# Kernel optimization log

Hardware: AMD Instinct MI355X
Metric: run time of the kernel (lower is better)

Reference implementation:

```python
import jax, jax.numpy as jnp
import numpy as np

N_NODES = 100000
N_EDGES = 500000
FEAT = 128
HID = 256
N_ETYPES = 249
N_LINKS = 16384


def _lin_init(key, out_dim, in_dim, bias=True):
    k1, k2 = jax.random.split(key)
    bound = 1.0 / np.sqrt(in_dim)
    w = jax.random.uniform(k1, (out_dim, in_dim), jnp.float32, -bound, bound)
    if bias:
        b = jax.random.uniform(k2, (out_dim,), jnp.float32, -bound, bound)
        return w, b
    return w


def setup_inputs() -> dict:
    key = jax.random.key(0)
    ks = jax.random.split(key, 24)
    x = jax.random.normal(ks[0], (N_NODES, FEAT), jnp.float32)
    edge_index = jax.random.randint(ks[1], (2, N_EDGES), 0, N_NODES, jnp.int64)
    edge_type = jax.random.randint(ks[2], (N_EDGES,), 0, N_ETYPES, jnp.int64)
    src_idx = jax.random.randint(ks[3], (N_LINKS,), 0, N_NODES, jnp.int64)
    dst_idx = jax.random.randint(ks[4], (N_LINKS,), 0, N_NODES, jnp.int64)

    w_emb, b_emb = _lin_init(ks[5], HID, FEAT)
    edge_table = jax.random.normal(ks[6], (N_ETYPES, HID), jnp.float32)
    wl0, bl0 = _lin_init(ks[7], HID, HID)
    wr0 = _lin_init(ks[8], HID, HID, bias=False)
    we0, be0 = _lin_init(ks[9], HID, HID)
    wl1, bl1 = _lin_init(ks[10], HID, HID)
    wr1 = _lin_init(ks[11], HID, HID, bias=False)
    we1, be1 = _lin_init(ks[12], HID, HID)
    wp1, bp1 = _lin_init(ks[13], HID, 4 * HID)
    wp2, bp2 = _lin_init(ks[14], 1, HID)
    return dict(x=x, edge_index=edge_index, edge_type=edge_type,
                src_idx=src_idx, dst_idx=dst_idx,
                w_emb=w_emb, b_emb=b_emb, edge_table=edge_table,
                wl0=wl0, bl0=bl0, wr0=wr0, we0=we0, be0=be0,
                wl1=wl1, bl1=bl1, wr1=wr1, we1=we1, be1=be1,
                wp1=wp1, bp1=bp1, wp2=wp2, bp2=bp2)


def _sage_layer(h, src, dst, deg, wl, bl, wr):
    # mean aggregation over incoming edges + self loop (add_self_loops)
    nb_sum = jax.ops.segment_sum(h[src], dst, num_segments=N_NODES)  # [N,H]
    mean = (nb_sum + h) / (deg + 1.0)[:, None]
    return mean @ wl.T + bl + h @ wr.T  # lin_l(mean) + lin_r(x)


def reference(x, edge_index, edge_type, src_idx, dst_idx,
              w_emb, b_emb, edge_table,
              wl0, bl0, wr0, we0, be0,
              wl1, bl1, wr1, we1, be1,
              wp1, bp1, wp2, bp2):
    src, dst = edge_index[0], edge_index[1]
    deg = jax.ops.segment_sum(jnp.ones((src.shape[0],), jnp.float32), dst,
                              num_segments=N_NODES)  # in-degree (no self loop)
    h = x @ w_emb.T + b_emb  # node_embedding
    edge_emb = edge_table[edge_type]  # [E,H]
    # edge_lin outputs are discarded by SAGEConv (matches torch behavior)
    _ = edge_emb @ we0.T + be0
    _ = edge_emb @ we1.T + be1
    h = jax.nn.relu(_sage_layer(h, src, dst, deg, wl0, bl0, wr0))
    h = jax.nn.relu(_sage_layer(h, src, dst, deg, wl1, bl1, wr1))
    s, d = h[src_idx], h[dst_idx]
    combined = jnp.concatenate([s, d, s * d, jnp.abs(s - d)], axis=1)  # [B,4H]
    hidden = jax.nn.relu(combined @ wp1.T + bp1)
    logits = hidden @ wp2.T + bp2  # [B,1]
    return jax.nn.sigmoid(logits).squeeze()
```

## Files before the change

kernel.cpp:

```cpp
#include <hip/hip_runtime.h>
#include <hip/hip_bf16.h>
#include <cstdint>
#include <type_traits>

#define N_NODES 100000
#define N_EDGES 500000
#define FEAT 128
#define HID 256
#define N_LINKS 16384
#define BCAP 32

typedef __attribute__((ext_vector_type(8))) short short8;
typedef __attribute__((ext_vector_type(4))) float floatx4;
typedef __attribute__((ext_vector_type(16))) float floatx16;

__device__ __forceinline__ float ldf(const float* p) { return *p; }
__device__ __forceinline__ float ldf(const __hip_bfloat16* p) { return __bfloat162float(*p); }
__device__ __forceinline__ void stf(float* p, float v) { *p = v; }
__device__ __forceinline__ void stf(__hip_bfloat16* p, float v) { *p = __float2bfloat16(v); }

__device__ __forceinline__ void load4(const __hip_bfloat16* p, float v[4]) {
    const uint2 q = *(const uint2*)p;
    v[0] = __uint_as_float(q.x << 16);
    v[1] = __uint_as_float(q.x & 0xffff0000u);
    v[2] = __uint_as_float(q.y << 16);
    v[3] = __uint_as_float(q.y & 0xffff0000u);
}
__device__ __forceinline__ void store4(__hip_bfloat16* p, const float v[4]) {
    __hip_bfloat16 b[4];
    b[0] = __float2bfloat16(v[0]); b[1] = __float2bfloat16(v[1]);
    b[2] = __float2bfloat16(v[2]); b[3] = __float2bfloat16(v[3]);
    *(uint2*)p = *(const uint2*)b;
}

__device__ __forceinline__ void load8(const __hip_bfloat16* p, float v[8]) {
    const uint4 q = *(const uint4*)p;
    v[0] = __uint_as_float(q.x << 16);
    v[1] = __uint_as_float(q.x & 0xffff0000u);
    v[2] = __uint_as_float(q.y << 16);
    v[3] = __uint_as_float(q.y & 0xffff0000u);
    v[4] = __uint_as_float(q.z << 16);
    v[5] = __uint_as_float(q.z & 0xffff0000u);
    v[6] = __uint_as_float(q.w << 16);
    v[7] = __uint_as_float(q.w & 0xffff0000u);
}
__device__ __forceinline__ void store8(__hip_bfloat16* p, const float v[8]) {
    __hip_bfloat16 b[8];
    #pragma unroll
    for (int i = 0; i < 8; i++) b[i] = __float2bfloat16(v[i]);
    *(uint4*)p = *(const uint4*)b;
}

__device__ __forceinline__ void unpack8(const uint4& q, float v[8]) {
    v[0] = __uint_as_float(q.x << 16);
    v[1] = __uint_as_float(q.x & 0xffff0000u);
    v[2] = __uint_as_float(q.y << 16);
    v[3] = __uint_as_float(q.y & 0xffff0000u);
    v[4] = __uint_as_float(q.z << 16);
    v[5] = __uint_as_float(q.z & 0xffff0000u);
    v[6] = __uint_as_float(q.w << 16);
    v[7] = __uint_as_float(q.w & 0xffff0000u);
}

__device__ __forceinline__ void acc8(const uint4& q, float a[8]) {
    a[0] += __uint_as_float(q.x << 16);
    a[1] += __uint_as_float(q.x & 0xffff0000u);
    a[2] += __uint_as_float(q.y << 16);
    a[3] += __uint_as_float(q.y & 0xffff0000u);
    a[4] += __uint_as_float(q.z << 16);
    a[5] += __uint_as_float(q.z & 0xffff0000u);
    a[6] += __uint_as_float(q.w << 16);
    a[7] += __uint_as_float(q.w & 0xffff0000u);
}

__device__ __forceinline__ void gload_lds16(const short* g, short* lds) {
    __builtin_amdgcn_global_load_lds(
        reinterpret_cast<const __attribute__((address_space(1))) unsigned int*>(
            reinterpret_cast<uintptr_t>(g)),
        reinterpret_cast<__attribute__((address_space(3))) unsigned int*>(
            reinterpret_cast<uintptr_t>(lds)),
        16, 0, 0);
}

__device__ __forceinline__ int clampi(int v, int n) { return ((unsigned)v < (unsigned)n) ? v : 0; }


__global__ void zero_f32(float* p, int n) {
    int i = blockIdx.x * blockDim.x + threadIdx.x;
    if (i < n) p[i] = 0.0f;
}

__global__ void init_misc(int* __restrict__ deg, int* __restrict__ h0pad,
                          int* __restrict__ h1pad) {
    int i = blockIdx.x * blockDim.x + threadIdx.x;
    if (i < N_NODES) deg[i] = 0;
    if (i < 128) { h0pad[i] = 0; h1pad[i] = 0; }
}

__global__ void cvt_x(const float4* __restrict__ x, __hip_bfloat16* __restrict__ xb, int n4) {
    int i = blockIdx.x * blockDim.x + threadIdx.x;
    if (i >= n4) return;
    float4 v = x[i];
    float a[4] = {v.x, v.y, v.z, v.w};
    store4(&xb[(size_t)i * 4], a);
}

#define POF_EMB 0
#define POF_L0  32768
#define POF_R0  98304
#define POF_L1  163840
#define POF_R1  229376
#define POF_P1  294912
#define WP_ALL  557056
__global__ void cvt_wall(const float* __restrict__ w_emb, const float* __restrict__ wl0,
                         const float* __restrict__ wr0, const float* __restrict__ wl1,
                         const float* __restrict__ wr1, const float* __restrict__ wp1,
                         __hip_bfloat16* __restrict__ wbp) {
    int i = blockIdx.x * blockDim.x + threadIdx.x;
    if (i >= WP_ALL) return;
    const float* src; int off, ks;
    if      (i < POF_L0) { src = w_emb; off = POF_EMB; ks = 128; }
    else if (i < POF_R0) { src = wl0;   off = POF_L0;  ks = 256; }
    else if (i < POF_L1) { src = wr0;   off = POF_R0;  ks = 256; }
    else if (i < POF_R1) { src = wl1;   off = POF_L1;  ks = 256; }
    else if (i < POF_P1) { src = wr1;   off = POF_R1;  ks = 256; }
    else                 { src = wp1;   off = POF_P1;  ks = 1024; }
    int o = i - off;
    int kseg = o >> 11;
    int rem  = o & 2047;
    int n = rem >> 3, j = rem & 7;
    wbp[i] = __float2bfloat16(src[n * ks + kseg * 8 + j]);
}


__global__ void fill_buckets(const int* __restrict__ src, const int* __restrict__ dst,
                             int* __restrict__ deg, int* __restrict__ ebuf, int nE) {
    int e = blockIdx.x * blockDim.x + threadIdx.x;
    if (e >= nE) return;
    int d = clampi(dst[e], N_NODES);
    int pos = atomicAdd(&deg[d], 1);
    if (pos < BCAP) ebuf[d * BCAP + pos] = clampi(src[e], N_NODES);
}

__global__ void sort_rows(const int* __restrict__ deg, int* __restrict__ ebuf) {
    int n = blockIdx.x * blockDim.x + threadIdx.x;
    if (n >= N_NODES) return;
    int dg = deg[n]; if (dg > BCAP) dg = BCAP;
    int start = n * BCAP, end = start + dg;
    for (int i = start + 1; i < end; i++) {
        int key = ebuf[i];
        int j = i - 1;
        while (j >= start && ebuf[j] > key) { ebuf[j + 1] = ebuf[j]; j--; }
        ebuf[j + 1] = key;
    }
}


__global__ __launch_bounds__(256) void gather_agg(const __hip_bfloat16* __restrict__ h,
                                                  const int* __restrict__ deg,
                                                  const int* __restrict__ ebuf,
                                                  __hip_bfloat16* __restrict__ agg) {
    int wave = threadIdx.x >> 6, lane = threadIdx.x & 63;
    int half = lane >> 5, l32 = lane & 31;
    int n = blockIdx.x * 8 + wave * 2 + half;
    bool active = (n < N_NODES);
    int nn = active ? n : 0;
    int dg = active ? deg[nn] : 0;
    int dgc = dg > BCAP ? BCAP : dg;
    int start = nn * BCAP;
    int end = start + dgc;

    float acc[8];
    {
        float sv[8];
        load8(&h[(long long)nn * HID + l32 * 8], sv);
        #pragma unroll
        for (int k = 0; k < 8; k++) acc[k] = sv[k];
    }

    for (int e = start; e < end; e += 8) {
        int cnt = end - e;
        uint4 raw[8];
        #pragma unroll
        for (int i = 0; i < 8; i++) {
            int t = e + i; t = (t < end) ? t : (end - 1);
            int idx = ebuf[t];
            int s = (i < cnt) ? idx : N_NODES;
            raw[i] = *(const uint4*)&h[(long long)s * HID + l32 * 8];
        }
        #pragma unroll
        for (int i = 0; i < 8; i++) acc8(raw[i], acc);
    }

    float inv = 1.0f / (float)(dg + 1);
    #pragma unroll
    for (int k = 0; k < 8; k++) acc[k] *= inv;
    if (active) store8(&agg[(long long)n * HID + l32 * 8], acc);
}


template <int KS, bool DUAL, typename TC, bool RELU>
__global__ __launch_bounds__(256, 2) void gemm_kc(const __hip_bfloat16* __restrict__ A1,
                                                  const __hip_bfloat16* __restrict__ A2,
                                                  const __hip_bfloat16* __restrict__ Bp1,
                                                  const __hip_bfloat16* __restrict__ Bp2,
                                                  const float* __restrict__ bias,
                                                  TC* __restrict__ C, int M, int GX) {
    const int N = 256;
    const int NSTEP = (DUAL ? 2 : 1) * KS / 64;
    __shared__ __align__(16) short As[2][128 * 64];
    __shared__ __align__(16) short Bs[2][64 * 128];

    const int tid = threadIdx.x;
    const int w = tid >> 6, lane = tid & 63;
    const int half = lane >> 5, l32 = lane & 31;
    const int cg = blockIdx.y;

    const short* A1s = (const short*)A1;
    const short* A2s = (const short*)A2;
    const short* B1s = (const short*)Bp1;
    const short* B2s = (const short*)Bp2;

    const int NT = (M + 127) / 128;
    for (int tile = blockIdx.x; tile < NT; tile += GX) {
        const int row0 = tile * 128;

        auto stage = [&](int buf, int t) {
            const short* Asrc; const short* Bsrc; int kl;
            if (!DUAL || t < KS / 64) { Asrc = A1s; Bsrc = B1s; kl = t * 64; }
            else                      { Asrc = A2s; Bsrc = B2s; kl = t * 64 - KS; }
            #pragma unroll
            for (int i = 0; i < 4; i++) {
                int idx = i * 256 + tid;
                int row = idx >> 3, b16 = idx & 7;
                int gr = row0 + row; if (gr >= M) gr = M - 1;
                gload_lds16(Asrc + (size_t)gr * KS + kl + ((b16 ^ (row & 7)) * 8),
                            (short*)&As[buf][idx * 8]);
            }
            #pragma unroll
            for (int i = 0; i < 4; i++) {
                int idx = i * 256 + tid;
                int kseg = idx >> 7, col = idx & 127;
                gload_lds16(Bsrc + ((size_t)((kl >> 3) + kseg) * 256 + cg * 128 + col) * 8,
                            (short*)&Bs[buf][idx * 8]);
            }
        };

        floatx16 acc[4] = {};
        int cur = 0;
        stage(0, 0);
        __syncthreads();

        for (int t = 0; t < NSTEP; t++) {
            if (t + 1 < NSTEP) stage(cur ^ 1, t + 1);

            const int arow = w * 32 + l32;
            #pragma unroll
            for (int k16 = 0; k16 < 4; k16++) {
                int e = k16 * 2 + half;
                short8 a = *(const short8*)&As[cur][(arow * 8 + (e ^ (l32 & 7))) * 8];
                #pragma unroll
                for (int ct = 0; ct < 4; ct++) {
                    short8 b = *(const short8*)&Bs[cur][(e * 128 + ct * 32 + l32) * 8];
                    acc[ct] = __builtin_amdgcn_mfma_f32_32x32x16_bf16(a, b, acc[ct], 0, 0, 0);
                }
            }
            __syncthreads();
            cur ^= 1;
        }

        #pragma unroll
        for (int ct = 0; ct < 4; ct++) {
            int c = cg * 128 + ct * 32 + l32;
            float bc = bias[c];
            #pragma unroll
            for (int reg = 0; reg < 16; reg++) {
                int rr = row0 + w * 32 + (reg & 3) + 8 * (reg >> 2) + 4 * half;
                if (rr < M) {
                    float v = acc[ct][reg] + bc;
                    if (RELU) v = fmaxf(v, 0.0f);
                    stf(&C[(size_t)rr * N + c], v);
                }
            }
        }
    }
}


__global__ __launch_bounds__(256, 3) void pred_gemm(const __hip_bfloat16* __restrict__ h,
                                                    const int* __restrict__ src_idx,
                                                    const int* __restrict__ dst_idx,
                                                    const __hip_bfloat16* __restrict__ Bp,
                                                    const float* __restrict__ bias,
                                                    float* __restrict__ C, int M) {
    const int N = 256;
    __shared__ __align__(16) short Bs[2][16 * 64 * 8];

    int w = threadIdx.x >> 6, lane = threadIdx.x & 63;
    int quad = lane >> 4, l16 = lane & 15;
    int cg = blockIdx.y;
    int row0 = blockIdx.x * 64 + w * 16;

    const short* Bps = (const short*)Bp;

    int rr = row0 + l16;
    int r = rr < M ? rr : M - 1;
    int sidx = clampi(src_idx[r], N_NODES);
    int didx = clampi(dst_idx[r], N_NODES);

    uint4 sraw[8], draw[8];
    #pragma unroll
    for (int j = 0; j < 8; j++) {
        sraw[j] = *(const uint4*)&h[(size_t)sidx * HID + quad * 8 + j * 32];
        draw[j] = *(const uint4*)&h[(size_t)didx * HID + quad * 8 + j * 32];
    }

    auto stageB = [&](int buf, int chunk) {
        #pragma unroll
        for (int i = 0; i < 4; i++) {
            int idx = i * 256 + (int)threadIdx.x;
            int ks = idx >> 6, col = idx & 63;
            gload_lds16(Bps + ((size_t)(chunk * 16 + ks) * 256 + cg * 64 + col) * 8,
                        (short*)&Bs[buf][idx * 8]);
        }
    };

    floatx4 acc[4] = {};
    stageB(0, 0);
    __syncthreads();
    int cur = 0;

    #pragma unroll
    for (int c = 0; c < 8; c++) {
        if (c + 1 < 8) stageB(cur ^ 1, c + 1);

        #pragma unroll
        for (int s = 0; s < 4; s++) {
            const int j = ((c & 1) ? 4 : 0) + s;
            short8 a;
            if (c < 2) {
                a = *(const short8*)&sraw[j];
            } else if (c < 4) {
                a = *(const short8*)&draw[j];
            } else {
                float sv[8], dv[8];
                unpack8(sraw[j], sv);
                unpack8(draw[j], dv);
                __hip_bfloat16 b8[8];
                if (c < 6) {
                    #pragma unroll
                    for (int q = 0; q < 8; q++) b8[q] = __float2bfloat16(sv[q] * dv[q]);
                } else {
                    #pragma unroll
                    for (int q = 0; q < 8; q++) b8[q] = __float2bfloat16(fabsf(sv[q] - dv[q]));
                }
                a = *(const short8*)b8;
            }
            #pragma unroll
            for (int ct = 0; ct < 4; ct++) {
                short8 b = *(const short8*)&Bs[cur][((s * 4 + quad) * 64 + ct * 16 + l16) * 8];
                acc[ct] = __builtin_amdgcn_mfma_f32_16x16x32_bf16(a, b, acc[ct], 0, 0, 0);
            }
        }
        __syncthreads();
        cur ^= 1;
    }

    #pragma unroll
    for (int ct = 0; ct < 4; ct++) {
        int c = cg * 64 + ct * 16 + l16;
        float bc = bias[c];
        #pragma unroll
        for (int i = 0; i < 4; i++) {
            int r2 = row0 + quad * 4 + i;
            if (r2 < M) C[(size_t)r2 * N + c] = fmaxf(acc[ct][i] + bc, 0.0f);
        }
    }
}

__global__ __launch_bounds__(256) void pred_final(const float* __restrict__ hidden,
                                                  const float* __restrict__ wp2,
                                                  const float* __restrict__ bp2,
                                                  float* __restrict__ out) {
    int wave = threadIdx.x >> 6;
    int lane = threadIdx.x & 63;
    int row = blockIdx.x * 4 + wave;
    if (row >= N_LINKS) return;
    const float4 hv = *(const float4*)&hidden[(long long)row * HID + lane * 4];
    const float4 wv = *(const float4*)&wp2[lane * 4];
    float v = hv.x * wv.x + hv.y * wv.y + hv.z * wv.z + hv.w * wv.w;
    #pragma unroll
    for (int off = 32; off > 0; off >>= 1) v += __shfl_down(v, off, 64);
    if (lane == 0) out[row] = 1.0f / (1.0f + expf(-(v + bp2[0])));
}


extern "C" void kernel_launch(void* const* d_in, const int* in_sizes, int n_in,
                              void* d_out, int out_size, void* d_ws, size_t ws_size,
                              hipStream_t stream) {
    const float* x          = (const float*)d_in[0];
    const int*   edge_index = (const int*)d_in[1];
    const int*   e_src      = edge_index;
    const int*   e_dst      = edge_index + N_EDGES;
    const int*   src_idx    = (const int*)d_in[3];
    const int*   dst_idx    = (const int*)d_in[4];
    const float* w_emb      = (const float*)d_in[5];
    const float* b_emb      = (const float*)d_in[6];
    const float* wl0        = (const float*)d_in[8];
    const float* bl0        = (const float*)d_in[9];
    const float* wr0        = (const float*)d_in[10];
    const float* wl1        = (const float*)d_in[13];
    const float* bl1        = (const float*)d_in[14];
    const float* wr1        = (const float*)d_in[15];
    const float* wp1        = (const float*)d_in[18];
    const float* bp1        = (const float*)d_in[19];
    const float* wp2        = (const float*)d_in[20];
    const float* bp2        = (const float*)d_in[21];
    float* out = (float*)d_out;

    typedef __hip_bfloat16 bf16;
    const size_t NH  = (size_t)N_NODES * HID;
    const size_t NH1 = (size_t)(N_NODES + 1) * HID;

    char* p = (char*)d_ws;
    bf16* h0   = (bf16*)p;  p += NH1 * 2;
    bf16* h1   = (bf16*)p;  p += NH1 * 2;
    bf16* agg  = (bf16*)p;  p += NH * 2;
    bf16* xb   = (bf16*)p;  p += (size_t)N_NODES * FEAT * 2;
    bf16* wbp  = (bf16*)p;  p += (size_t)WP_ALL * 2;
    p = (char*)(((uintptr_t)p + 255) & ~(uintptr_t)255);
    int* deg  = (int*)p; p += (size_t)N_NODES * 4;
    int* ebuf = (int*)p; p += (size_t)N_NODES * BCAP * 4;
    const size_t need = (size_t)(p - (char*)d_ws);

    if (ws_size < need) {
        zero_f32<<<(out_size + 255) / 256, 256, 0, stream>>>(out, out_size);
        return;
    }

    float* hidden = (float*)h1;

    init_misc<<<(N_NODES + 255) / 256, 256, 0, stream>>>(
        deg, (int*)(h0 + NH), (int*)(h1 + NH));
    fill_buckets<<<(N_EDGES + 255) / 256, 256, 0, stream>>>(e_src, e_dst, deg, ebuf, N_EDGES);
    sort_rows<<<(N_NODES + 255) / 256, 256, 0, stream>>>(deg, ebuf);

    cvt_x<<<((N_NODES * FEAT / 4) + 255) / 256, 256, 0, stream>>>((const float4*)x, xb, N_NODES * FEAT / 4);
    cvt_wall<<<(WP_ALL + 255) / 256, 256, 0, stream>>>(
        w_emb, wl0, wr0, wl1, wr1, wp1, wbp);

    const int GX = 256;
    dim3 pgrid(GX, 2);

    gemm_kc<128, false, bf16, false><<<pgrid, 256, 0, stream>>>(
        xb, nullptr, wbp + POF_EMB, nullptr, b_emb, h0, N_NODES, GX);

    gather_agg<<<(N_NODES + 7) / 8, 256, 0, stream>>>(h0, deg, ebuf, agg);
    gemm_kc<256, true, bf16, true><<<pgrid, 256, 0, stream>>>(
        agg, h0, wbp + POF_L0, wbp + POF_R0, bl0, h1, N_NODES, GX);

    gather_agg<<<(N_NODES + 7) / 8, 256, 0, stream>>>(h1, deg, ebuf, agg);
    gemm_kc<256, true, bf16, true><<<pgrid, 256, 0, stream>>>(
        agg, h1, wbp + POF_L1, wbp + POF_R1, bl1, h0, N_NODES, GX);

    dim3 pgrid2(N_LINKS / 64, 4);
    pred_gemm<<<pgrid2, 256, 0, stream>>>(
        h0, src_idx, dst_idx, wbp + POF_P1, bp1, hidden, N_LINKS);
    pred_final<<<N_LINKS / 4, 256, 0, stream>>>(hidden, wp2, bp2, out);
}
```

Baseline: 436.4 us.

## Fuse prep kernels into one launch and halve GEMM K-tile for higher occupancy

Merges init_misc, cvt_x and cvt_wall into a single prep_all launch that selects its work by block index, removing two kernel launches. The node GEMMs drop their K step from 64 to 32, halving LDS per block, and raise launch bounds to four blocks per CU. Smaller K tiles mean twice as many pipeline steps and barriers per tile, which may offset the occupancy gain. The grid stays at 256x2 blocks, so extra occupancy only helps if blocks were limited per CU.

Measured after the change: 479.4 us. 9.9% more time.

```diff
diff --git a/kernel.cpp b/kernel.cpp
--- a/kernel.cpp
+++ b/kernel.cpp
@@ -90,21 +90,6 @@
     if (i < n) p[i] = 0.0f;
 }
 
-__global__ void init_misc(int* __restrict__ deg, int* __restrict__ h0pad,
-                          int* __restrict__ h1pad) {
-    int i = blockIdx.x * blockDim.x + threadIdx.x;
-    if (i < N_NODES) deg[i] = 0;
-    if (i < 128) { h0pad[i] = 0; h1pad[i] = 0; }
-}
-
-__global__ void cvt_x(const float4* __restrict__ x, __hip_bfloat16* __restrict__ xb, int n4) {
-    int i = blockIdx.x * blockDim.x + threadIdx.x;
-    if (i >= n4) return;
-    float4 v = x[i];
-    float a[4] = {v.x, v.y, v.z, v.w};
-    store4(&xb[(size_t)i * 4], a);
-}
-
 #define POF_EMB 0
 #define POF_L0  32768
 #define POF_R0  98304
@@ -112,24 +97,44 @@
 #define POF_R1  229376
 #define POF_P1  294912
 #define WP_ALL  557056
-__global__ void cvt_wall(const float* __restrict__ w_emb, const float* __restrict__ wl0,
+
+#define CVTX_NB 12500
+#define INIT_NB ((N_NODES + 255) / 256)
+#define CVTW_NB (WP_ALL / 256)
+__global__ void prep_all(const float4* __restrict__ x, __hip_bfloat16* __restrict__ xb,
+                         int* __restrict__ deg, int* __restrict__ h0pad,
+                         int* __restrict__ h1pad,
+                         const float* __restrict__ w_emb, const float* __restrict__ wl0,
                          const float* __restrict__ wr0, const float* __restrict__ wl1,
                          const float* __restrict__ wr1, const float* __restrict__ wp1,
                          __hip_bfloat16* __restrict__ wbp) {
-    int i = blockIdx.x * blockDim.x + threadIdx.x;
-    if (i >= WP_ALL) return;
-    const float* src; int off, ks;
-    if      (i < POF_L0) { src = w_emb; off = POF_EMB; ks = 128; }
-    else if (i < POF_R0) { src = wl0;   off = POF_L0;  ks = 256; }
-    else if (i < POF_L1) { src = wr0;   off = POF_R0;  ks = 256; }
-    else if (i < POF_R1) { src = wl1;   off = POF_L1;  ks = 256; }
-    else if (i < POF_P1) { src = wr1;   off = POF_R1;  ks = 256; }
-    else                 { src = wp1;   off = POF_P1;  ks = 1024; }
-    int o = i - off;
-    int kseg = o >> 11;
-    int rem  = o & 2047;
-    int n = rem >> 3, j = rem & 7;
-    wbp[i] = __float2bfloat16(src[n * ks + kseg * 8 + j]);
+    int b = blockIdx.x;
+    if (b < CVTX_NB) {
+        int i = b * 256 + threadIdx.x;
+        float4 v = x[i];
+        float a[4] = {v.x, v.y, v.z, v.w};
+        store4(&xb[(size_t)i * 4], a);
+    } else if (b < CVTX_NB + INIT_NB) {
+        int i = (b - CVTX_NB) * 256 + threadIdx.x;
+        if (i < N_NODES) deg[i] = 0;
+        if (i < 128) { h0pad[i] = 0; h1pad[i] = 0; }
+    } else {
+        int i = (b - CVTX_NB - INIT_NB) * 256 + threadIdx.x;
+        if (i < WP_ALL) {
+            const float* src; int off, ks;
+            if      (i < POF_L0) { src = w_emb; off = POF_EMB; ks = 128; }
+            else if (i < POF_R0) { src = wl0;   off = POF_L0;  ks = 256; }
+            else if (i < POF_L1) { src = wr0;   off = POF_R0;  ks = 256; }
+            else if (i < POF_R1) { src = wl1;   off = POF_L1;  ks = 256; }
+            else if (i < POF_P1) { src = wr1;   off = POF_R1;  ks = 256; }
+            else                 { src = wp1;   off = POF_P1;  ks = 1024; }
+            int o = i - off;
+            int kseg = o >> 11;
+            int rem  = o & 2047;
+            int n = rem >> 3, j = rem & 7;
+            wbp[i] = __float2bfloat16(src[n * ks + kseg * 8 + j]);
+        }
+    }
 }
 
 
@@ -200,16 +205,16 @@
 
 
 template <int KS, bool DUAL, typename TC, bool RELU>
-__global__ __launch_bounds__(256, 2) void gemm_kc(const __hip_bfloat16* __restrict__ A1,
+__global__ __launch_bounds__(256, 4) void gemm_kc(const __hip_bfloat16* __restrict__ A1,
                                                   const __hip_bfloat16* __restrict__ A2,
                                                   const __hip_bfloat16* __restrict__ Bp1,
                                                   const __hip_bfloat16* __restrict__ Bp2,
                                                   const float* __restrict__ bias,
                                                   TC* __restrict__ C, int M, int GX) {
     const int N = 256;
-    const int NSTEP = (DUAL ? 2 : 1) * KS / 64;
-    __shared__ __align__(16) short As[2][128 * 64];
-    __shared__ __align__(16) short Bs[2][64 * 128];
+    const int NSTEP = (DUAL ? 2 : 1) * KS / 32;
+    __shared__ __align__(16) short As[2][128 * 32];
+    __shared__ __align__(16) short Bs[2][32 * 128];
 
     const int tid = threadIdx.x;
     const int w = tid >> 6, lane = tid & 63;
@@ -227,18 +232,18 @@
 
         auto stage = [&](int buf, int t) {
             const short* Asrc; const short* Bsrc; int kl;
-            if (!DUAL || t < KS / 64) { Asrc = A1s; Bsrc = B1s; kl = t * 64; }
-            else                      { Asrc = A2s; Bsrc = B2s; kl = t * 64 - KS; }
+            if (!DUAL || t < KS / 32) { Asrc = A1s; Bsrc = B1s; kl = t * 32; }
+            else                      { Asrc = A2s; Bsrc = B2s; kl = t * 32 - KS; }
             #pragma unroll
-            for (int i = 0; i < 4; i++) {
+            for (int i = 0; i < 2; i++) {
                 int idx = i * 256 + tid;
-                int row = idx >> 3, b16 = idx & 7;
+                int row = idx >> 2, b16 = idx & 3;
                 int gr = row0 + row; if (gr >= M) gr = M - 1;
-                gload_lds16(Asrc + (size_t)gr * KS + kl + ((b16 ^ (row & 7)) * 8),
+                gload_lds16(Asrc + (size_t)gr * KS + kl + ((b16 ^ (row & 3)) * 8),
                             (short*)&As[buf][idx * 8]);
             }
             #pragma unroll
-            for (int i = 0; i < 4; i++) {
+            for (int i = 0; i < 2; i++) {
                 int idx = i * 256 + tid;
                 int kseg = idx >> 7, col = idx & 127;
                 gload_lds16(Bsrc + ((size_t)((kl >> 3) + kseg) * 256 + cg * 128 + col) * 8,
@@ -256,9 +261,9 @@
 
             const int arow = w * 32 + l32;
             #pragma unroll
-            for (int k16 = 0; k16 < 4; k16++) {
+            for (int k16 = 0; k16 < 2; k16++) {
                 int e = k16 * 2 + half;
-                short8 a = *(const short8*)&As[cur][(arow * 8 + (e ^ (l32 & 7))) * 8];
+                short8 a = *(const short8*)&As[cur][(arow * 4 + (e ^ (l32 & 3))) * 8];
                 #pragma unroll
                 for (int ct = 0; ct < 4; ct++) {
                     short8 b = *(const short8*)&Bs[cur][(e * 128 + ct * 32 + l32) * 8];
@@ -440,14 +445,12 @@
 
     float* hidden = (float*)h1;
 
-    init_misc<<<(N_NODES + 255) / 256, 256, 0, stream>>>(
-        deg, (int*)(h0 + NH), (int*)(h1 + NH));
+    prep_all<<<CVTX_NB + INIT_NB + CVTW_NB, 256, 0, stream>>>(
+        (const float4*)x, xb, deg, (int*)(h0 + NH), (int*)(h1 + NH),
+        w_emb, wl0, wr0, wl1, wr1, wp1, wbp);
+
     fill_buckets<<<(N_EDGES + 255) / 256, 256, 0, stream>>>(e_src, e_dst, deg, ebuf, N_EDGES);
     sort_rows<<<(N_NODES + 255) / 256, 256, 0, stream>>>(deg, ebuf);
-
-    cvt_x<<<((N_NODES * FEAT / 4) + 255) / 256, 256, 0, stream>>>((const float4*)x, xb, N_NODES * FEAT / 4);
-    cvt_wall<<<(WP_ALL + 255) / 256, 256, 0, stream>>>(
-        w_emb, wl0, wr0, wl1, wr1, wp1, wbp);
 
     const int GX = 256;
     dim3 pgrid(GX, 2);
```
